# Performance work log

Hardware: AMD Instinct MI355X
Metric: run time of the kernel (lower is better)

Reference implementation:

```python
import jax, jax.numpy as jnp
import numpy as np

H = 32          # num_attention_heads
HD = 128        # head_dim
HID = H * HD    # hidden_size = 4096
KB_LEN = 1024   # number of KB entries
TOPK = 128      # top_k_kb (dynamic_sparsify=True)
ROPE_THETA = 10000.0
PAD = -1000000000.0  # PADDING_VALUE


def rope_cos_sin(position_ids, head_dim, theta):
    inv_freq = 1.0 / (theta ** (jnp.arange(0, head_dim, 2, dtype=jnp.float32) / head_dim))
    freqs = position_ids.astype(jnp.float32)[..., None] * inv_freq  # [B,q,hd/2]
    emb = jnp.concatenate([freqs, freqs], axis=-1)                  # [B,q,hd]
    return jnp.cos(emb), jnp.sin(emb)


def rotate_half(x):
    half = x.shape[-1] // 2
    return jnp.concatenate([-x[..., half:], x[..., :half]], axis=-1)


def apply_rope(q, k, cos, sin):
    cos = cos[:, None]  # [B,1,q,hd]
    sin = sin[:, None]
    return q * cos + rotate_half(q) * sin, k * cos + rotate_half(k) * sin


def setup_inputs() -> dict:
    key = jax.random.key(0)
    ks = jax.random.split(key, 9)
    B, Q = 1, 2048
    w_scale = 0.02  # keep activations numerically sane
    hidden_states = jax.random.normal(ks[0], (B, Q, HID), jnp.float32)
    causal = jnp.where(jnp.tril(jnp.ones((Q, Q), bool)), 0.0, PAD).astype(jnp.float32)
    attention_mask = jnp.broadcast_to(causal[None, None], (B, 1, Q, Q))
    position_ids = jnp.broadcast_to(jnp.arange(Q)[None], (B, Q))
    kb_keys = jax.random.normal(ks[1], (KB_LEN, HID), jnp.float32)
    kb_values = jax.random.normal(ks[2], (KB_LEN, HID), jnp.float32)
    Wq = jax.random.normal(ks[3], (HID, HID), jnp.float32) * w_scale
    Wq2 = jax.random.normal(ks[4], (HID, HID), jnp.float32) * w_scale
    Wk = jax.random.normal(ks[5], (HID, HID), jnp.float32) * w_scale
    Wv = jax.random.normal(ks[6], (HID, HID), jnp.float32) * w_scale
    Wo = jax.random.normal(ks[7], (HID, HID), jnp.float32) * w_scale
    score_shift = jnp.zeros((H, 1), jnp.float32) - 3.0
    return {"hidden_states": hidden_states, "attention_mask": attention_mask,
            "position_ids": position_ids, "kb_keys": kb_keys, "kb_values": kb_values,
            "Wq": Wq, "Wq2": Wq2, "Wk": Wk, "Wv": Wv, "Wo": Wo,
            "score_shift": score_shift}


def kblam_attention(hidden_states, attention_mask, position_ids, kb_keys, kb_values,
                    Wq, Wq2, Wk, Wv, Wo, score_shift):
    B, Q, _ = hidden_states.shape
    scale = 1.0 / np.sqrt(HD)

    def heads(x):  # [B,Q,HID] -> [B,H,Q,HD]
        return x.reshape(B, Q, H, HD).transpose(0, 2, 1, 3)

    q = heads(hidden_states @ Wq.T)
    q2 = heads(hidden_states @ Wq2.T)   # second query head (used for KB top-k pruning)
    k = heads(hidden_states @ Wk.T)
    v = heads(hidden_states @ Wv.T)

    cos, sin = rope_cos_sin(position_ids, HD, ROPE_THETA)
    q, k = apply_rope(q, k, cos, sin)   # num_kv_groups == 1, repeat_kv is identity

    # --- KB path: [kb_len, H*HD] -> [B,H,kb_len,HD] ---
    kbk = jnp.broadcast_to(kb_keys.reshape(KB_LEN, H, HD).transpose(1, 0, 2)[None], (B, H, KB_LEN, HD))
    kbv = jnp.broadcast_to(kb_values.reshape(KB_LEN, H, HD).transpose(1, 0, 2)[None], (B, H, KB_LEN, HD))

    # prune_key_value (dynamic_sparsify): top-k KB rows by summed q2-scores
    aw2 = jnp.einsum('bhqd,bhkd->bhqk', q2, kbk) * scale          # [B,H,Q,KB_LEN]
    idx = jax.lax.stop_gradient(jax.lax.top_k(aw2.sum((1, 2)), TOPK)[1])  # [B,TOPK]
    gidx = jnp.broadcast_to(idx[:, None, :, None], (B, H, TOPK, HD))
    kbk = jnp.take_along_axis(kbk, gidx, axis=2)                  # [B,H,TOPK,HD]
    kbv = jnp.take_along_axis(kbv, gidx, axis=2)
    kb_len = TOPK

    k_all = jnp.concatenate([kbk, k], axis=2)                     # [B,H,kb_len+Q,HD]
    v_all = jnp.concatenate([kbv, v], axis=2)

    # kb attention mask: zeros, except fully-padded query rows get PADDING_VALUE
    padding_mask = jnp.all(attention_mask < 0, axis=-1, keepdims=True)  # [B,1,Q,1]
    kb_mask = jnp.where(padding_mask, PAD, 0.0).astype(attention_mask.dtype)
    mask = jnp.concatenate([jnp.broadcast_to(kb_mask, (B, 1, Q, kb_len)), attention_mask], axis=-1)

    attn = jnp.einsum('bhqd,bhkd->bhqk', q, k_all) * scale
    # learned per-head shift on KB scores (score_shift: [H,1], init -3)
    attn = attn.at[..., :kb_len].add(score_shift.reshape(1, H, 1, 1))
    attn = attn + mask
    attn = jax.nn.softmax(attn.astype(jnp.float32), axis=-1).astype(q.dtype)

    out = jnp.einsum('bhqk,bhkd->bhqd', attn, v_all)              # [B,H,Q,HD]
    out = out.transpose(0, 2, 1, 3).reshape(B, Q, HID)
    return out @ Wo.T


def reference(hidden_states, attention_mask, position_ids, kb_keys, kb_values,
              Wq, Wq2, Wk, Wv, Wo, score_shift):
    return kblam_attention(hidden_states, attention_mask, position_ids, kb_keys, kb_values,
                           Wq, Wq2, Wk, Wv, Wo, score_shift)
```

## Files before the change

### kernel.cpp

```cpp
#include <hip/hip_runtime.h>
#include <stdint.h>
#include <stddef.h>

#define NH 32
#define HD 128
#define HID 4096
#define QLEN 2048
#define KBLEN 1024
#define NTOPK 128
#define KVLEN 2176
#define PADV -1e9f
#define SCALE 0.08838834764831845f
#define LOG2E 1.4426950408889634f
#define SC2 (SCALE * LOG2E)
#define DEFER_THR 8.0f

typedef __attribute__((ext_vector_type(4))) float f32x4;
typedef __attribute__((ext_vector_type(4))) unsigned short u16x4;
typedef __attribute__((ext_vector_type(8))) short s16x8;

typedef const __attribute__((address_space(1))) void* gas1_t;
typedef __attribute__((address_space(3))) void* las3_t;

__device__ __forceinline__ void gload_lds16(const void* g, void* l) {
  __builtin_amdgcn_global_load_lds((gas1_t)g, (las3_t)l, 16, 0, 0);
}

__device__ __forceinline__ unsigned short f2bf(float x) {
  union { float f; unsigned u; } z; z.f = x;
  unsigned r = z.u + 0x7fffu + ((z.u >> 16) & 1u);
  return (unsigned short)(r >> 16);
}


__global__ void k_cast(const float* __restrict__ src, unsigned short* __restrict__ dst, int n4) {
  int i = blockIdx.x * 256 + threadIdx.x;
  if (i >= n4) return;
  f32x4 v = ((const f32x4*)src)[i];
  u16x4 o;
  o[0] = f2bf(v[0]); o[1] = f2bf(v[1]); o[2] = f2bf(v[2]); o[3] = f2bf(v[3]);
  ((u16x4*)dst)[i] = o;
}

__global__ void k_rowsum_p(const float* __restrict__ x, float* __restrict__ part) {
  int d = blockIdx.x * 256 + threadIdx.x;
  int q0 = blockIdx.y * 128;
  float acc = 0.f;
  for (int q = q0; q < q0 + 128; ++q) acc += x[(size_t)q * HID + d];
  part[(size_t)blockIdx.y * HID + d] = acc;
}
__global__ void k_rowsum_r(const float* __restrict__ part, float* __restrict__ out) {
  int d = blockIdx.x * 256 + threadIdx.x;
  float acc = 0.f;
#pragma unroll
  for (int i = 0; i < 16; ++i) acc += part[(size_t)i * HID + d];
  out[d] = acc;
}

__global__ void k_dotrows(const float* __restrict__ vec, const float* __restrict__ mat,
                          float* __restrict__ out, int K, float s) {
  int n = blockIdx.x * 4 + (threadIdx.x >> 6);
  int lane = threadIdx.x & 63;
  const float* row = mat + (size_t)n * K;
  float acc = 0.f;
  for (int j = lane; j < K; j += 64) acc += vec[j] * row[j];
#pragma unroll
  for (int off = 32; off > 0; off >>= 1) acc += __shfl_down(acc, off, 64);
  if (lane == 0) out[n] = acc * s;
}

__global__ void k_topk(const float* __restrict__ scores, int* __restrict__ idx) {
  __shared__ float s[KBLEN];
  int t = threadIdx.x;
  s[t] = scores[t];
  __syncthreads();
  float mine = s[t];
  int rank = 0;
  for (int j = 0; j < KBLEN; ++j) {
    float v = s[j];
    rank += (v > mine) || (v == mine && j < t);
  }
  if (rank < NTOPK) idx[rank] = t;
}

__global__ void k_cs(const int* __restrict__ pos_ids, float2* __restrict__ cs) {
  int t = blockIdx.x * 256 + threadIdx.x;
  int p = t >> 6, i = t & 63;
  float pos = (float)pos_ids[p];
  float invf = powf(10000.0f, -(float)i / 64.0f);
  float a = pos * invf;
  cs[p * 64 + i] = make_float2(cosf(a), sinf(a));
}

__global__ void k_gather(const float* __restrict__ kbk, const float* __restrict__ kbv,
                         const int* __restrict__ idx,
                         unsigned short* __restrict__ kall, unsigned short* __restrict__ vallT) {
  int t = blockIdx.x * 256 + threadIdx.x;
  int d = t & 127;
  int i = (t >> 7) & 127;
  int hh = t >> 14;
  int kr = idx[i];
  size_t src = (size_t)kr * HID + hh * HD + d;
  kall[((size_t)hh * KVLEN + i) * HD + d] = f2bf(kbk[src]);
  vallT[((size_t)hh * HD + d) * KVLEN + i] = f2bf(kbv[src]);
}

#define GBK 64
#define ABUF 8192
#define BBUF 16384
#define BUFE (ABUF + BBUF)

template<int MODE>
__global__ __launch_bounds__(512)
void gemm_bt(const unsigned short* __restrict__ A, const unsigned short* __restrict__ B,
             float* __restrict__ Cf, unsigned short* __restrict__ Cb,
             int M, int N, int K, int RH, int RO, const float2* __restrict__ cs2,
             float qsc) {
  __shared__ unsigned short lds[3 * BUFE];
  const int tid = threadIdx.x;
  const int lane = tid & 63;
  const int wave = tid >> 6;
  const int lo = lane & 15, hi = lane >> 4;
  const int wm = wave >> 2, wn = wave & 3;

  const int nwg = gridDim.x * gridDim.y;
  const int orig = blockIdx.y * gridDim.x + blockIdx.x;
  const int wg = (orig & 7) * (nwg >> 3) + (orig >> 3);
  const int bx = wg % gridDim.x, by = wg / gridDim.x;
  const int m0 = by * 128, n0 = bx * 256;

  auto stageA = [&](int kt, int bufe, int g) {
    int j0 = g * 512 + wave * 64;
    int j = j0 + lane;
    int row = j >> 3, cb = j & 7;
    gload_lds16(A + (size_t)(m0 + row) * K + kt * GBK + ((cb ^ (row & 7)) << 3),
                (void*)(lds + bufe + j0 * 8));
  };
  auto stageB = [&](int kt, int bufe, int g) {
    int j0 = g * 512 + wave * 64;
    int j = j0 + lane;
    int row = j >> 3, cb = j & 7;
    gload_lds16(B + (size_t)(n0 + row) * K + kt * GBK + ((cb ^ (row & 7)) << 3),
                (void*)(lds + bufe + ABUF + j0 * 8));
  };

  f32x4 acc[4][4] = {};

  stageA(0, 0, 0); stageA(0, 0, 1);
  stageB(0, 0, 0); stageB(0, 0, 1); stageB(0, 0, 2); stageB(0, 0, 3);
  stageA(1, BUFE, 0); stageA(1, BUFE, 1);
  stageB(1, BUFE, 0); stageB(1, BUFE, 1); stageB(1, BUFE, 2); stageB(1, BUFE, 3);

  const int NT = K / GBK;
  const int sa = (lo & 7) << 3;
  const int bbase = (wn >> 1) * 128 + (wn & 1) * 32;
  int bi = 0;

  for (int kt = 0; kt < NT; ++kt) {
    if (kt < NT - 1) { asm volatile("s_waitcnt vmcnt(6)" ::: "memory"); }
    else             { asm volatile("s_waitcnt vmcnt(0)" ::: "memory"); }
    __builtin_amdgcn_sched_barrier(0);
    __builtin_amdgcn_s_barrier();
    __builtin_amdgcn_sched_barrier(0);

    const int bufe = bi * BUFE;
    const int nbufe = ((bi + 2 >= 3) ? bi - 1 : bi + 2) * BUFE;
    const bool pre = (kt + 2 < NT);
    const unsigned short* Ab = lds + bufe;
    const unsigned short* Bb = lds + bufe + ABUF;
    const int arow = wm * 64 + lo;
    const int brow = bbase + lo;

    s16x8 af[4], b01[2], b23[2];
    const int c0 = (hi * 8) ^ sa;
    const int c1 = (32 + hi * 8) ^ sa;

#pragma unroll
    for (int i = 0; i < 4; ++i) af[i] = *(const s16x8*)(Ab + (arow + i * 16) * 64 + c0);
    b01[0] = *(const s16x8*)(Bb + (brow +  0) * 64 + c0);
    b01[1] = *(const s16x8*)(Bb + (brow + 16) * 64 + c0);
    if (pre) { stageA(kt + 2, nbufe, 0); stageA(kt + 2, nbufe, 1); }
    asm volatile("s_waitcnt lgkmcnt(0)" ::: "memory");
    __builtin_amdgcn_sched_barrier(0);
    __builtin_amdgcn_s_setprio(1);
#pragma unroll
    for (int i = 0; i < 4; ++i) {
      acc[i][0] = __builtin_amdgcn_mfma_f32_16x16x32_bf16(af[i], b01[0], acc[i][0], 0, 0, 0);
      acc[i][1] = __builtin_amdgcn_mfma_f32_16x16x32_bf16(af[i], b01[1], acc[i][1], 0, 0, 0);
    }
    __builtin_amdgcn_s_setprio(0);

    b23[0] = *(const s16x8*)(Bb + (brow + 64) * 64 + c0);
    b23[1] = *(const s16x8*)(Bb + (brow + 80) * 64 + c0);
    if (pre) { stageB(kt + 2, nbufe, 0); stageB(kt + 2, nbufe, 1); }
    asm volatile("s_waitcnt lgkmcnt(0)" ::: "memory");
    __builtin_amdgcn_sched_barrier(0);
    __builtin_amdgcn_s_setprio(1);
#pragma unroll
    for (int i = 0; i < 4; ++i) {
      acc[i][2] = __builtin_amdgcn_mfma_f32_16x16x32_bf16(af[i], b23[0], acc[i][2], 0, 0, 0);
      acc[i][3] = __builtin_amdgcn_mfma_f32_16x16x32_bf16(af[i], b23[1], acc[i][3], 0, 0, 0);
    }
    __builtin_amdgcn_s_setprio(0);

#pragma unroll
    for (int i = 0; i < 4; ++i) af[i] = *(const s16x8*)(Ab + (arow + i * 16) * 64 + c1);
    b01[0] = *(const s16x8*)(Bb + (brow +  0) * 64 + c1);
    b01[1] = *(const s16x8*)(Bb + (brow + 16) * 64 + c1);
    if (pre) { stageB(kt + 2, nbufe, 2); stageB(kt + 2, nbufe, 3); }
    asm volatile("s_waitcnt lgkmcnt(0)" ::: "memory");
    __builtin_amdgcn_sched_barrier(0);
    __builtin_amdgcn_s_setprio(1);
#pragma unroll
    for (int i = 0; i < 4; ++i) {
      acc[i][0] = __builtin_amdgcn_mfma_f32_16x16x32_bf16(af[i], b01[0], acc[i][0], 0, 0, 0);
      acc[i][1] = __builtin_amdgcn_mfma_f32_16x16x32_bf16(af[i], b01[1], acc[i][1], 0, 0, 0);
    }
    __builtin_amdgcn_s_setprio(0);

    b23[0] = *(const s16x8*)(Bb + (brow + 64) * 64 + c1);
    b23[1] = *(const s16x8*)(Bb + (brow + 80) * 64 + c1);
    asm volatile("s_waitcnt lgkmcnt(0)" ::: "memory");
    __builtin_amdgcn_sched_barrier(0);
    __builtin_amdgcn_s_setprio(1);
#pragma unroll
    for (int i = 0; i < 4; ++i) {
      acc[i][2] = __builtin_amdgcn_mfma_f32_16x16x32_bf16(af[i], b23[0], acc[i][2], 0, 0, 0);
      acc[i][3] = __builtin_amdgcn_mfma_f32_16x16x32_bf16(af[i], b23[1], acc[i][3], 0, 0, 0);
    }
    __builtin_amdgcn_s_setprio(0);

    bi = (bi + 1 == 3) ? 0 : bi + 1;
  }

  if (MODE == 2) {
#pragma unroll
    for (int i = 0; i < 4; ++i) {
#pragma unroll
      for (int j = 0; j < 2; ++j) {
#pragma unroll
        for (int r = 0; r < 4; ++r) {
          int row = m0 + wm * 64 + i * 16 + hi * 4 + r;
          int col = n0 + bbase + j * 16 + lo;
          int hh = col >> 7, d = col & 127;
          float2 cp = cs2[row * 64 + d];
          float x1 = acc[i][j][r] * qsc, x2 = acc[i][j + 2][r] * qsc;
          size_t base = ((size_t)hh * RH + RO + row) * HD;
          Cb[base + d]      = f2bf(x1 * cp.x - x2 * cp.y);
          Cb[base + d + 64] = f2bf(x2 * cp.x + x1 * cp.y);
        }
      }
    }
  } else if (MODE == 3) {
#pragma unroll
    for (int i = 0; i < 4; ++i) {
#pragma unroll
      for (int j = 0; j < 4; ++j) {
        int rowb = m0 + wm * 64 + i * 16 + hi * 4;
        int col = n0 + bbase + (j >> 1) * 64 + (j & 1) * 16 + lo;
        int hh = col >> 7, d = col & 127;
        u16x4 o4;
#pragma unroll
        for (int r = 0; r < 4; ++r) o4[r] = f2bf(acc[i][j][r]);
        *(u16x4*)(Cb + ((size_t)hh * HD + d) * RH + RO + rowb) = o4;
      }
    }
  } else {
#pragma unroll
    for (int i = 0; i < 4; ++i) {
#pragma unroll
      for (int j = 0; j < 4; ++j) {
#pragma unroll
        for (int r = 0; r < 4; ++r) {
          int row = m0 + wm * 64 + i * 16 + hi * 4 + r;
          int col = n0 + bbase + (j >> 1) * 64 + (j & 1) * 16 + lo;
          float v = acc[i][j][r];
          if (MODE == 0) {
            Cf[(size_t)row * N + col] = v;
          } else {
            int hh = col >> 7, d = col & 127;
            Cb[((size_t)hh * RH + RO + row) * HD + d] = f2bf(v);
          }
        }
      }
    }
  }
}

__global__ __launch_bounds__(256)
void attn_kernel(const unsigned short* __restrict__ qh,
                 const unsigned short* __restrict__ kall,
                 const unsigned short* __restrict__ vallT,
                 const float* __restrict__ sshift,
                 unsigned short* __restrict__ ctx) {
  __shared__ __align__(1024) unsigned short Ks[64 * 128];
  __shared__ __align__(1024) unsigned short Vs[128 * 64];
  __shared__ __align__(16)  unsigned short Plds[4][16 * 72];

  int orig = blockIdx.y * 32 + blockIdx.x;
  int wgid = (orig & 7) * 128 + (orig >> 3);
  int h = wgid >> 5;
  int qc = 31 - (wgid & 31);

  const int tid = threadIdx.x;
  const int lane = tid & 63;
  const int wave = tid >> 6;
  const int lo = lane & 15;
  const int hi = lane >> 4;
  const float shiftL = sshift[h] * LOG2E;

  const unsigned short* kb = kall + (size_t)h * KVLEN * HD;
  const unsigned short* vtb = vallT + (size_t)h * HD * KVLEN;

  const int m0 = qc * 64;
  const int nt = qc + 3;
  const int qrow = m0 + wave * 16 + hi * 4;

  s16x8 qf[4];
  {
    const unsigned short* qp = qh + ((size_t)h * QLEN + m0 + wave * 16 + lo) * HD + hi * 8;
#pragma unroll
    for (int kc = 0; kc < 4; ++kc) qf[kc] = *(const s16x8*)(qp + kc * 32);
  }

  float m_run[4], l_part[4];
#pragma unroll
  for (int r = 0; r < 4; ++r) { m_run[r] = -1e30f; l_part[r] = 0.f; }
  f32x4 o[8] = {};

  for (int kt = 0; kt < nt; ++kt) {
    const unsigned short* kg = kb + (size_t)kt * 64 * HD;
    const unsigned short* vg = vtb + kt * 64;
    __syncthreads();
#pragma unroll
    for (int it = 0; it < 4; ++it) {
      int j0 = it * 256 + wave * 64;
      int j = j0 + lane;
      int row = j >> 4, cb = j & 15;
      gload_lds16(kg + row * 128 + ((cb ^ (row & 7)) * 8), (void*)(Ks + j0 * 8));
      int d = j >> 3, c = j & 7;
      gload_lds16(vg + (size_t)d * KVLEN + ((c ^ (d & 7)) << 3), (void*)(Vs + j0 * 8));
    }
    __syncthreads();

    f32x4 s[4] = {};
#pragma unroll
    for (int kc = 0; kc < 4; ++kc) {
#pragma unroll
      for (int g = 0; g < 4; ++g) {
        int key = g * 16 + lo;
        s16x8 kf = *(const s16x8*)(Ks + key * 128 + (((kc * 4 + hi) ^ (key & 7)) * 8));
        s[g] = __builtin_amdgcn_mfma_f32_16x16x32_bf16(qf[kc], kf, s[g], 0, 0, 0);
      }
    }

    if (kt < 2) {
#pragma unroll
      for (int g = 0; g < 4; ++g)
#pragma unroll
        for (int r = 0; r < 4; ++r) s[g][r] += shiftL;
    } else if (kt == nt - 1) {
      const int kvbase = kt * 64;
#pragma unroll
      for (int r = 0; r < 4; ++r) {
        int qr = qrow + r;
#pragma unroll
        for (int g = 0; g < 4; ++g) {
          int kv = kvbase + g * 16 + lo;
          s[g][r] = (kv - NTOPK > qr) ? PADV : s[g][r];
        }
      }
    }

    float mx[4];
    bool need = false;
#pragma unroll
    for (int r = 0; r < 4; ++r) {
      mx[r] = fmaxf(fmaxf(s[0][r], s[1][r]), fmaxf(s[2][r], s[3][r]));
      need = need || (mx[r] > m_run[r] + DEFER_THR);
    }
    if (__any((int)need)) {
#pragma unroll
      for (int off = 1; off < 16; off <<= 1)
#pragma unroll
        for (int r = 0; r < 4; ++r) mx[r] = fmaxf(mx[r], __shfl_xor(mx[r], off, 64));
#pragma unroll
      for (int r = 0; r < 4; ++r) {
        float mn = fmaxf(m_run[r], mx[r]);
        float alpha = __builtin_amdgcn_exp2f(m_run[r] - mn);
        m_run[r] = mn;
        l_part[r] *= alpha;
#pragma unroll
        for (int db = 0; db < 8; ++db) o[db][r] *= alpha;
      }
    }

#pragma unroll
    for (int r = 0; r < 4; ++r) {
#pragma unroll
      for (int g = 0; g < 4; ++g) {
        float p = __builtin_amdgcn_exp2f(s[g][r] - m_run[r]);
        l_part[r] += p;
        Plds[wave][(hi * 4 + r) * 72 + g * 16 + lo] = f2bf(p);
      }
    }

    s16x8 pf0 = *(const s16x8*)(&Plds[wave][lo * 72 + hi * 8]);
    s16x8 pf1 = *(const s16x8*)(&Plds[wave][lo * 72 + 32 + hi * 8]);
#pragma unroll
    for (int db = 0; db < 8; ++db) {
      int d = db * 16 + lo;
      s16x8 vf0 = *(const s16x8*)(Vs + d * 64 + ((hi       ^ (d & 7)) << 3));
      s16x8 vf1 = *(const s16x8*)(Vs + d * 64 + (((4 + hi) ^ (d & 7)) << 3));
      o[db] = __builtin_amdgcn_mfma_f32_16x16x32_bf16(pf0, vf0, o[db], 0, 0, 0);
      o[db] = __builtin_amdgcn_mfma_f32_16x16x32_bf16(pf1, vf1, o[db], 0, 0, 0);
    }
  }

#pragma unroll
  for (int off = 1; off < 16; off <<= 1)
#pragma unroll
    for (int r = 0; r < 4; ++r) l_part[r] += __shfl_xor(l_part[r], off, 64);

  float rinv[4];
#pragma unroll
  for (int r = 0; r < 4; ++r) rinv[r] = __builtin_amdgcn_rcpf(l_part[r]);

#pragma unroll
  for (int db = 0; db < 8; ++db) {
#pragma unroll
    for (int r = 0; r < 4; ++r) {
      int row = qrow + r;
      int col = h * HD + db * 16 + lo;
      ctx[(size_t)row * HID + col] = f2bf(o[db][r] * rinv[r]);
    }
  }
}


extern "C" void kernel_launch(void* const* d_in, const int* in_sizes, int n_in,
                              void* d_out, int out_size, void* d_ws, size_t ws_size,
                              hipStream_t stream) {
  const float* hidden    = (const float*)d_in[0];
  const int*   pos       = (const int*)d_in[2];
  const float* kb_keys   = (const float*)d_in[3];
  const float* kb_values = (const float*)d_in[4];
  const float* Wq        = (const float*)d_in[5];
  const float* Wq2       = (const float*)d_in[6];
  const float* Wk        = (const float*)d_in[7];
  const float* Wv        = (const float*)d_in[8];
  const float* Wo        = (const float*)d_in[9];
  const float* sshift    = (const float*)d_in[10];
  float* out = (float*)d_out;

  char* ws = (char*)d_ws;
  size_t off = 0;
  auto alloc = [&](size_t bytes) { char* p = ws + off; off += (bytes + 255) & ~(size_t)255; return p; };
  unsigned short* hidden_bf = (unsigned short*)alloc((size_t)QLEN * HID * 2);
  unsigned short* wbuf      = (unsigned short*)alloc((size_t)HID * HID * 2);
  unsigned short* qbf       = (unsigned short*)alloc((size_t)NH * QLEN * HD * 2);
  unsigned short* kallp     = (unsigned short*)alloc((size_t)NH * KVLEN * HD * 2);
  unsigned short* vallT     = (unsigned short*)alloc((size_t)NH * HD * KVLEN * 2);
  unsigned short* ctx       = (unsigned short*)alloc((size_t)QLEN * HID * 2);
  float2*         cs2       = (float2*)alloc((size_t)QLEN * 64 * 8);
  float*          part      = (float*)alloc((size_t)16 * HID * 4);
  float*          hsum      = (float*)alloc(HID * 4);
  float*          qs        = (float*)alloc(HID * 4);
  float*          scores    = (float*)alloc(KBLEN * 4);
  int*            idx       = (int*)alloc(NTOPK * 4);

  dim3 blk(256);

  k_cast<<<QLEN * HID / 4 / 256, blk, 0, stream>>>(hidden, hidden_bf, QLEN * HID / 4);
  k_rowsum_p<<<dim3(HID / 256, 16), blk, 0, stream>>>(hidden, part);
  k_rowsum_r<<<HID / 256, blk, 0, stream>>>(part, hsum);
  k_dotrows<<<HID / 4, blk, 0, stream>>>(hsum, Wq2, qs, HID, 1.0f);
  k_dotrows<<<KBLEN / 4, blk, 0, stream>>>(qs, kb_keys, scores, HID, SCALE);
  k_topk<<<1, KBLEN, 0, stream>>>(scores, idx);
  k_cs<<<QLEN * 64 / 256, blk, 0, stream>>>(pos, cs2);

  dim3 ggrid(HID / 256, QLEN / 128);
  dim3 gblk(512);
  int wcast_blocks = HID * HID / 4 / 256;

  k_cast<<<wcast_blocks, blk, 0, stream>>>(Wq, wbuf, HID * HID / 4);
  gemm_bt<2><<<ggrid, gblk, 0, stream>>>(hidden_bf, wbuf, nullptr, qbf, QLEN, HID, HID, QLEN, 0, cs2, (float)SC2);
  k_cast<<<wcast_blocks, blk, 0, stream>>>(Wk, wbuf, HID * HID / 4);
  gemm_bt<2><<<ggrid, gblk, 0, stream>>>(hidden_bf, wbuf, nullptr, kallp, QLEN, HID, HID, KVLEN, NTOPK, cs2, 1.0f);
  k_cast<<<wcast_blocks, blk, 0, stream>>>(Wv, wbuf, HID * HID / 4);
  gemm_bt<3><<<ggrid, gblk, 0, stream>>>(hidden_bf, wbuf, nullptr, vallT, QLEN, HID, HID, KVLEN, NTOPK, cs2, 1.0f);

  k_gather<<<NH * NTOPK * HD / 256, blk, 0, stream>>>(kb_keys, kb_values, idx, kallp, vallT);

  dim3 agrid(32, NH);
  attn_kernel<<<agrid, blk, 0, stream>>>(qbf, kallp, vallT, sshift, ctx);

  k_cast<<<wcast_blocks, blk, 0, stream>>>(Wo, wbuf, HID * HID / 4);
  gemm_bt<0><<<ggrid, gblk, 0, stream>>>(ctx, wbuf, out, nullptr, QLEN, HID, HID, 0, 0, cs2, 1.0f);
}
```

Before: 566.3 us.

## Double attention query tile per block to 128 rows, two row groups per wave

The attention kernel now processes 128 query rows per workgroup instead of 64. Each wave handles two 16-row groups, so every K/V tile loaded into LDS is reused by twice as many query rows, halving global K/V traffic and barrier count per query. Waves skip diagonal tiles that are fully masked for them, and the P scratch buffer gets an XOR swizzle to reduce LDS bank conflicts. The trade-off is half as many workgroups (512), more registers per wave that may lower occupancy, and worse load balance across the causal triangle.

```diff
diff --git a/kernel.cpp b/kernel.cpp
--- a/kernel.cpp
+++ b/kernel.cpp
@@ -295,12 +295,12 @@
                  unsigned short* __restrict__ ctx) {
   __shared__ __align__(1024) unsigned short Ks[64 * 128];
   __shared__ __align__(1024) unsigned short Vs[128 * 64];
-  __shared__ __align__(16)  unsigned short Plds[4][16 * 72];
-
-  int orig = blockIdx.y * 32 + blockIdx.x;
-  int wgid = (orig & 7) * 128 + (orig >> 3);
-  int h = wgid >> 5;
-  int qc = 31 - (wgid & 31);
+  __shared__ __align__(16)  unsigned short Plds[4][32 * 72];
+
+  int orig = blockIdx.y * 16 + blockIdx.x;
+  int wgid = (orig & 7) * 64 + (orig >> 3);
+  int h = wgid >> 4;
+  int qc = 15 - (wgid & 15);
 
   const int tid = threadIdx.x;
   const int lane = tid & 63;
@@ -312,21 +312,26 @@
   const unsigned short* kb = kall + (size_t)h * KVLEN * HD;
   const unsigned short* vtb = vallT + (size_t)h * HD * KVLEN;
 
-  const int m0 = qc * 64;
-  const int nt = qc + 3;
-  const int qrow = m0 + wave * 16 + hi * 4;
-
-  s16x8 qf[4];
-  {
-    const unsigned short* qp = qh + ((size_t)h * QLEN + m0 + wave * 16 + lo) * HD + hi * 8;
-#pragma unroll
-    for (int kc = 0; kc < 4; ++kc) qf[kc] = *(const s16x8*)(qp + kc * 32);
+  const int m0 = qc * 128;
+  const int nt = 2 * qc + 4;
+  const int diagkt = nt - 2 + (wave >> 1);
+
+  s16x8 qf[2][4];
+#pragma unroll
+  for (int qg = 0; qg < 2; ++qg) {
+    const unsigned short* qp = qh + ((size_t)h * QLEN + m0 + wave * 32 + qg * 16 + lo) * HD + hi * 8;
+#pragma unroll
+    for (int kc = 0; kc < 4; ++kc) qf[qg][kc] = *(const s16x8*)(qp + kc * 32);
   }
 
-  float m_run[4], l_part[4];
-#pragma unroll
-  for (int r = 0; r < 4; ++r) { m_run[r] = -1e30f; l_part[r] = 0.f; }
-  f32x4 o[8] = {};
+  float m_run[2][4], l_part[2][4];
+#pragma unroll
+  for (int qg = 0; qg < 2; ++qg)
+#pragma unroll
+    for (int r = 0; r < 4; ++r) { m_run[qg][r] = -1e30f; l_part[qg][r] = 0.f; }
+  f32x4 o[2][8] = {};
+
+  const int rkey = ((lo >> 2) & 3) << 4;
 
   for (int kt = 0; kt < nt; ++kt) {
     const unsigned short* kg = kb + (size_t)kt * 64 * HD;
@@ -334,105 +339,137 @@
     __syncthreads();
 #pragma unroll
     for (int it = 0; it < 4; ++it) {
-      int j0 = it * 256 + wave * 64;
-      int j = j0 + lane;
+      int j0 = it * 256 + tid - lane + lane;
+      int j = it * 256 + tid;
+      int jw = it * 256 + wave * 64;
       int row = j >> 4, cb = j & 15;
-      gload_lds16(kg + row * 128 + ((cb ^ (row & 7)) * 8), (void*)(Ks + j0 * 8));
+      gload_lds16(kg + row * 128 + ((cb ^ (row & 7)) * 8), (void*)(Ks + jw * 8));
       int d = j >> 3, c = j & 7;
-      gload_lds16(vg + (size_t)d * KVLEN + ((c ^ (d & 7)) << 3), (void*)(Vs + j0 * 8));
+      gload_lds16(vg + (size_t)d * KVLEN + ((c ^ (d & 7)) << 3), (void*)(Vs + jw * 8));
+      (void)j0;
     }
     __syncthreads();
 
-    f32x4 s[4] = {};
-#pragma unroll
-    for (int kc = 0; kc < 4; ++kc) {
-#pragma unroll
-      for (int g = 0; g < 4; ++g) {
-        int key = g * 16 + lo;
-        s16x8 kf = *(const s16x8*)(Ks + key * 128 + (((kc * 4 + hi) ^ (key & 7)) * 8));
-        s[g] = __builtin_amdgcn_mfma_f32_16x16x32_bf16(qf[kc], kf, s[g], 0, 0, 0);
-      }
-    }
-
-    if (kt < 2) {
-#pragma unroll
-      for (int g = 0; g < 4; ++g)
-#pragma unroll
-        for (int r = 0; r < 4; ++r) s[g][r] += shiftL;
-    } else if (kt == nt - 1) {
-      const int kvbase = kt * 64;
+    if (kt <= diagkt) {
+      f32x4 s[2][4] = {};
+#pragma unroll
+      for (int kc = 0; kc < 4; ++kc) {
+#pragma unroll
+        for (int kgi = 0; kgi < 4; ++kgi) {
+          int key = kgi * 16 + lo;
+          s16x8 kf = *(const s16x8*)(Ks + key * 128 + (((kc * 4 + hi) ^ (key & 7)) * 8));
+          s[0][kgi] = __builtin_amdgcn_mfma_f32_16x16x32_bf16(qf[0][kc], kf, s[0][kgi], 0, 0, 0);
+          s[1][kgi] = __builtin_amdgcn_mfma_f32_16x16x32_bf16(qf[1][kc], kf, s[1][kgi], 0, 0, 0);
+        }
+      }
+
+      if (kt < 2) {
+#pragma unroll
+        for (int qg = 0; qg < 2; ++qg)
+#pragma unroll
+          for (int kgi = 0; kgi < 4; ++kgi)
+#pragma unroll
+            for (int r = 0; r < 4; ++r) s[qg][kgi][r] += shiftL;
+      } else if (kt >= nt - 2) {
+        const int kvbase = kt * 64 - NTOPK;
+#pragma unroll
+        for (int qg = 0; qg < 2; ++qg) {
+#pragma unroll
+          for (int r = 0; r < 4; ++r) {
+            int qr = m0 + wave * 32 + qg * 16 + hi * 4 + r;
+#pragma unroll
+            for (int kgi = 0; kgi < 4; ++kgi) {
+              int kv = kvbase + kgi * 16 + lo;
+              s[qg][kgi][r] = (kv > qr) ? PADV : s[qg][kgi][r];
+            }
+          }
+        }
+      }
+
+      float mx[2][4];
+      bool need = false;
+#pragma unroll
+      for (int qg = 0; qg < 2; ++qg)
+#pragma unroll
+        for (int r = 0; r < 4; ++r) {
+          mx[qg][r] = fmaxf(fmaxf(s[qg][0][r], s[qg][1][r]), fmaxf(s[qg][2][r], s[qg][3][r]));
+          need = need || (mx[qg][r] > m_run[qg][r] + DEFER_THR);
+        }
+      if (__any((int)need)) {
+#pragma unroll
+        for (int off = 1; off < 16; off <<= 1)
+#pragma unroll
+          for (int qg = 0; qg < 2; ++qg)
+#pragma unroll
+            for (int r = 0; r < 4; ++r) mx[qg][r] = fmaxf(mx[qg][r], __shfl_xor(mx[qg][r], off, 64));
+#pragma unroll
+        for (int qg = 0; qg < 2; ++qg)
+#pragma unroll
+          for (int r = 0; r < 4; ++r) {
+            float mn = fmaxf(m_run[qg][r], mx[qg][r]);
+            float alpha = __builtin_amdgcn_exp2f(m_run[qg][r] - mn);
+            m_run[qg][r] = mn;
+            l_part[qg][r] *= alpha;
+#pragma unroll
+            for (int db = 0; db < 8; ++db) o[qg][db][r] *= alpha;
+          }
+      }
+
+#pragma unroll
+      for (int qg = 0; qg < 2; ++qg) {
+#pragma unroll
+        for (int r = 0; r < 4; ++r) {
+#pragma unroll
+          for (int kgi = 0; kgi < 4; ++kgi) {
+            float p = __builtin_amdgcn_exp2f(s[qg][kgi][r] - m_run[qg][r]);
+            l_part[qg][r] += p;
+            Plds[wave][(qg * 16 + hi * 4 + r) * 72 + ((kgi * 16 + lo) ^ (hi << 4))] = f2bf(p);
+          }
+        }
+      }
+
+      s16x8 pf[2][2];
+#pragma unroll
+      for (int qg = 0; qg < 2; ++qg) {
+        pf[qg][0] = *(const s16x8*)(&Plds[wave][(qg * 16 + lo) * 72 + ((hi * 8) ^ rkey)]);
+        pf[qg][1] = *(const s16x8*)(&Plds[wave][(qg * 16 + lo) * 72 + ((32 + hi * 8) ^ rkey)]);
+      }
+#pragma unroll
+      for (int db = 0; db < 8; ++db) {
+        int d = db * 16 + lo;
+        s16x8 vf0 = *(const s16x8*)(Vs + d * 64 + ((hi       ^ (d & 7)) << 3));
+        s16x8 vf1 = *(const s16x8*)(Vs + d * 64 + (((4 + hi) ^ (d & 7)) << 3));
+        o[0][db] = __builtin_amdgcn_mfma_f32_16x16x32_bf16(pf[0][0], vf0, o[0][db], 0, 0, 0);
+        o[0][db] = __builtin_amdgcn_mfma_f32_16x16x32_bf16(pf[0][1], vf1, o[0][db], 0, 0, 0);
+        o[1][db] = __builtin_amdgcn_mfma_f32_16x16x32_bf16(pf[1][0], vf0, o[1][db], 0, 0, 0);
+        o[1][db] = __builtin_amdgcn_mfma_f32_16x16x32_bf16(pf[1][1], vf1, o[1][db], 0, 0, 0);
+      }
+    }
+  }
+
+#pragma unroll
+  for (int off = 1; off < 16; off <<= 1)
+#pragma unroll
+    for (int qg = 0; qg < 2; ++qg)
+#pragma unroll
+      for (int r = 0; r < 4; ++r) l_part[qg][r] += __shfl_xor(l_part[qg][r], off, 64);
+
+  float rinv[2][4];
+#pragma unroll
+  for (int qg = 0; qg < 2; ++qg)
+#pragma unroll
+    for (int r = 0; r < 4; ++r) rinv[qg][r] = __builtin_amdgcn_rcpf(l_part[qg][r]);
+
+#pragma unroll
+  for (int qg = 0; qg < 2; ++qg) {
+#pragma unroll
+    for (int db = 0; db < 8; ++db) {
 #pragma unroll
       for (int r = 0; r < 4; ++r) {
-        int qr = qrow + r;
-#pragma unroll
-        for (int g = 0; g < 4; ++g) {
-          int kv = kvbase + g * 16 + lo;
-          s[g][r] = (kv - NTOPK > qr) ? PADV : s[g][r];
-        }
-      }
-    }
-
-    float mx[4];
-    bool need = false;
-#pragma unroll
-    for (int r = 0; r < 4; ++r) {
-      mx[r] = fmaxf(fmaxf(s[0][r], s[1][r]), fmaxf(s[2][r], s[3][r]));
-      need = need || (mx[r] > m_run[r] + DEFER_THR);
-    }
-    if (__any((int)need)) {
-#pragma unroll
-      for (int off = 1; off < 16; off <<= 1)
-#pragma unroll
-        for (int r = 0; r < 4; ++r) mx[r] = fmaxf(mx[r], __shfl_xor(mx[r], off, 64));
-#pragma unroll
-      for (int r = 0; r < 4; ++r) {
-        float mn = fmaxf(m_run[r], mx[r]);
-        float alpha = __builtin_amdgcn_exp2f(m_run[r] - mn);
-        m_run[r] = mn;
-        l_part[r] *= alpha;
-#pragma unroll
-        for (int db = 0; db < 8; ++db) o[db][r] *= alpha;
-      }
-    }
-
-#pragma unroll
-    for (int r = 0; r < 4; ++r) {
-#pragma unroll
-      for (int g = 0; g < 4; ++g) {
-        float p = __builtin_amdgcn_exp2f(s[g][r] - m_run[r]);
-        l_part[r] += p;
-        Plds[wave][(hi * 4 + r) * 72 + g * 16 + lo] = f2bf(p);
-      }
-    }
-
-    s16x8 pf0 = *(const s16x8*)(&Plds[wave][lo * 72 + hi * 8]);
-    s16x8 pf1 = *(const s16x8*)(&Plds[wave][lo * 72 + 32 + hi * 8]);
-#pragma unroll
-    for (int db = 0; db < 8; ++db) {
-      int d = db * 16 + lo;
-      s16x8 vf0 = *(const s16x8*)(Vs + d * 64 + ((hi       ^ (d & 7)) << 3));
-      s16x8 vf1 = *(const s16x8*)(Vs + d * 64 + (((4 + hi) ^ (d & 7)) << 3));
-      o[db] = __builtin_amdgcn_mfma_f32_16x16x32_bf16(pf0, vf0, o[db], 0, 0, 0);
-      o[db] = __builtin_amdgcn_mfma_f32_16x16x32_bf16(pf1, vf1, o[db], 0, 0, 0);
-    }
-  }
-
-#pragma unroll
-  for (int off = 1; off < 16; off <<= 1)
-#pragma unroll
-    for (int r = 0; r < 4; ++r) l_part[r] += __shfl_xor(l_part[r], off, 64);
-
-  float rinv[4];
-#pragma unroll
-  for (int r = 0; r < 4; ++r) rinv[r] = __builtin_amdgcn_rcpf(l_part[r]);
-
-#pragma unroll
-  for (int db = 0; db < 8; ++db) {
-#pragma unroll
-    for (int r = 0; r < 4; ++r) {
-      int row = qrow + r;
-      int col = h * HD + db * 16 + lo;
-      ctx[(size_t)row * HID + col] = f2bf(o[db][r] * rinv[r]);
+        int row = m0 + wave * 32 + qg * 16 + hi * 4 + r;
+        int col = h * HD + db * 16 + lo;
+        ctx[(size_t)row * HID + col] = f2bf(o[qg][db][r] * rinv[qg][r]);
+      }
     }
   }
 }
@@ -492,7 +529,7 @@
 
   k_gather<<<NH * NTOPK * HD / 256, blk, 0, stream>>>(kb_keys, kb_values, idx, kallp, vallT);
 
-  dim3 agrid(32, NH);
+  dim3 agrid(16, NH);
   attn_kernel<<<agrid, blk, 0, stream>>>(qbf, kallp, vallT, sshift, ctx);
 
   k_cast<<<wcast_blocks, blk, 0, stream>>>(Wo, wbuf, HID * HID / 4);
```

Result: slower. 604.7 us (+6.8%).

## Fuse fp32-to-bf16 weight cast into GEMM B-operand staging

Applied to the files above, without the earlier changes.

Removes the four separate weight-cast kernels. The GEMM now reads fp32 weights directly through registers, packs them to bf16 with v_cvt_pk_bf16_f32, and writes them into LDS, pipelined one k-tile ahead. This drops a full write and re-read of each 32 MB bf16 weight copy. In exchange, the GEMM reads twice the B bytes from global memory, uses more registers, replaces async LDS DMA with VGPR round-trips, and changes the vmcnt accounting.

```diff
diff --git a/kernel.cpp b/kernel.cpp
--- a/kernel.cpp
+++ b/kernel.cpp
@@ -17,6 +17,7 @@
 
 typedef __attribute__((ext_vector_type(4))) float f32x4;
 typedef __attribute__((ext_vector_type(4))) unsigned short u16x4;
+typedef __attribute__((ext_vector_type(4))) unsigned u32x4;
 typedef __attribute__((ext_vector_type(8))) short s16x8;
 
 typedef const __attribute__((address_space(1))) void* gas1_t;
@@ -30,6 +31,12 @@
   union { float f; unsigned u; } z; z.f = x;
   unsigned r = z.u + 0x7fffu + ((z.u >> 16) & 1u);
   return (unsigned short)(r >> 16);
+}
+
+__device__ __forceinline__ unsigned cvt_pk_bf16(float s0, float s1) {
+  unsigned d;
+  asm volatile("v_cvt_pk_bf16_f32 %0, %1, %2" : "=v"(d) : "v"(s0), "v"(s1));
+  return d;
 }
 
 
@@ -112,7 +119,7 @@
 
 template<int MODE>
 __global__ __launch_bounds__(512)
-void gemm_bt(const unsigned short* __restrict__ A, const unsigned short* __restrict__ B,
+void gemm_bt(const unsigned short* __restrict__ A, const float* __restrict__ B,
              float* __restrict__ Cf, unsigned short* __restrict__ Cb,
              int M, int N, int K, int RH, int RO, const float2* __restrict__ cs2,
              float qsc) {
@@ -136,20 +143,39 @@
     gload_lds16(A + (size_t)(m0 + row) * K + kt * GBK + ((cb ^ (row & 7)) << 3),
                 (void*)(lds + bufe + j0 * 8));
   };
-  auto stageB = [&](int kt, int bufe, int g) {
-    int j0 = g * 512 + wave * 64;
-    int j = j0 + lane;
-    int row = j >> 3, cb = j & 7;
-    gload_lds16(B + (size_t)(n0 + row) * K + kt * GBK + ((cb ^ (row & 7)) << 3),
-                (void*)(lds + bufe + ABUF + j0 * 8));
+
+  f32x4 breg[8];
+  auto loadB = [&](int kt) {
+#pragma unroll
+    for (int c = 0; c < 4; ++c) {
+      int j = tid * 4 + c;
+      int row = j >> 3, cb = j & 7;
+      const float* src = B + (size_t)(n0 + row) * K + kt * GBK + ((cb ^ (row & 7)) << 3);
+      breg[c * 2]     = *(const f32x4*)(src);
+      breg[c * 2 + 1] = *(const f32x4*)(src + 4);
+    }
   };
+  auto writeB = [&](int bufe, int c) {
+    int j = tid * 4 + c;
+    u32x4 u;
+    f32x4 v0 = breg[c * 2], v1 = breg[c * 2 + 1];
+    u[0] = cvt_pk_bf16(v0[0], v0[1]);
+    u[1] = cvt_pk_bf16(v0[2], v0[3]);
+    u[2] = cvt_pk_bf16(v1[0], v1[1]);
+    u[3] = cvt_pk_bf16(v1[2], v1[3]);
+    *(u32x4*)(lds + bufe + ABUF + j * 8) = u;
+  };
 
   f32x4 acc[4][4] = {};
 
+  loadB(0);
   stageA(0, 0, 0); stageA(0, 0, 1);
-  stageB(0, 0, 0); stageB(0, 0, 1); stageB(0, 0, 2); stageB(0, 0, 3);
+  asm volatile("s_waitcnt vmcnt(2)" ::: "memory");
+#pragma unroll
+  for (int c = 0; c < 4; ++c) writeB(0, c);
   stageA(1, BUFE, 0); stageA(1, BUFE, 1);
-  stageB(1, BUFE, 0); stageB(1, BUFE, 1); stageB(1, BUFE, 2); stageB(1, BUFE, 3);
+  loadB(1);
+  asm volatile("s_waitcnt lgkmcnt(0)" ::: "memory");
 
   const int NT = K / GBK;
   const int sa = (lo & 7) << 3;
@@ -157,15 +183,16 @@
   int bi = 0;
 
   for (int kt = 0; kt < NT; ++kt) {
-    if (kt < NT - 1) { asm volatile("s_waitcnt vmcnt(6)" ::: "memory"); }
-    else             { asm volatile("s_waitcnt vmcnt(0)" ::: "memory"); }
+    asm volatile("s_waitcnt vmcnt(10)" ::: "memory");
     __builtin_amdgcn_sched_barrier(0);
     __builtin_amdgcn_s_barrier();
     __builtin_amdgcn_sched_barrier(0);
 
     const int bufe = bi * BUFE;
-    const int nbufe = ((bi + 2 >= 3) ? bi - 1 : bi + 2) * BUFE;
+    const int nbufe  = ((bi + 2 >= 3) ? bi - 1 : bi + 2) * BUFE;
+    const int wbufe  = ((bi + 1 >= 3) ? bi - 2 : bi + 1) * BUFE;
     const bool pre = (kt + 2 < NT);
+    const bool wnext = (kt + 1 < NT);
     const unsigned short* Ab = lds + bufe;
     const unsigned short* Bb = lds + bufe + ABUF;
     const int arow = wm * 64 + lo;
@@ -180,6 +207,7 @@
     b01[0] = *(const s16x8*)(Bb + (brow +  0) * 64 + c0);
     b01[1] = *(const s16x8*)(Bb + (brow + 16) * 64 + c0);
     if (pre) { stageA(kt + 2, nbufe, 0); stageA(kt + 2, nbufe, 1); }
+    if (wnext) { writeB(wbufe, 0); writeB(wbufe, 1); }
     asm volatile("s_waitcnt lgkmcnt(0)" ::: "memory");
     __builtin_amdgcn_sched_barrier(0);
     __builtin_amdgcn_s_setprio(1);
@@ -192,7 +220,7 @@
 
     b23[0] = *(const s16x8*)(Bb + (brow + 64) * 64 + c0);
     b23[1] = *(const s16x8*)(Bb + (brow + 80) * 64 + c0);
-    if (pre) { stageB(kt + 2, nbufe, 0); stageB(kt + 2, nbufe, 1); }
+    if (wnext) { writeB(wbufe, 2); writeB(wbufe, 3); }
     asm volatile("s_waitcnt lgkmcnt(0)" ::: "memory");
     __builtin_amdgcn_sched_barrier(0);
     __builtin_amdgcn_s_setprio(1);
@@ -207,7 +235,7 @@
     for (int i = 0; i < 4; ++i) af[i] = *(const s16x8*)(Ab + (arow + i * 16) * 64 + c1);
     b01[0] = *(const s16x8*)(Bb + (brow +  0) * 64 + c1);
     b01[1] = *(const s16x8*)(Bb + (brow + 16) * 64 + c1);
-    if (pre) { stageB(kt + 2, nbufe, 2); stageB(kt + 2, nbufe, 3); }
+    if (pre) loadB(kt + 2);
     asm volatile("s_waitcnt lgkmcnt(0)" ::: "memory");
     __builtin_amdgcn_sched_barrier(0);
     __builtin_amdgcn_s_setprio(1);
@@ -457,7 +485,6 @@
   size_t off = 0;
   auto alloc = [&](size_t bytes) { char* p = ws + off; off += (bytes + 255) & ~(size_t)255; return p; };
   unsigned short* hidden_bf = (unsigned short*)alloc((size_t)QLEN * HID * 2);
-  unsigned short* wbuf      = (unsigned short*)alloc((size_t)HID * HID * 2);
   unsigned short* qbf       = (unsigned short*)alloc((size_t)NH * QLEN * HD * 2);
   unsigned short* kallp     = (unsigned short*)alloc((size_t)NH * KVLEN * HD * 2);
   unsigned short* vallT     = (unsigned short*)alloc((size_t)NH * HD * KVLEN * 2);
@@ -481,20 +508,15 @@
 
   dim3 ggrid(HID / 256, QLEN / 128);
   dim3 gblk(512);
-  int wcast_blocks = HID * HID / 4 / 256;
-
-  k_cast<<<wcast_blocks, blk, 0, stream>>>(Wq, wbuf, HID * HID / 4);
-  gemm_bt<2><<<ggrid, gblk, 0, stream>>>(hidden_bf, wbuf, nullptr, qbf, QLEN, HID, HID, QLEN, 0, cs2, (float)SC2);
-  k_cast<<<wcast_blocks, blk, 0, stream>>>(Wk, wbuf, HID * HID / 4);
-  gemm_bt<2><<<ggrid, gblk, 0, stream>>>(hidden_bf, wbuf, nullptr, kallp, QLEN, HID, HID, KVLEN, NTOPK, cs2, 1.0f);
-  k_cast<<<wcast_blocks, blk, 0, stream>>>(Wv, wbuf, HID * HID / 4);
-  gemm_bt<3><<<ggrid, gblk, 0, stream>>>(hidden_bf, wbuf, nullptr, vallT, QLEN, HID, HID, KVLEN, NTOPK, cs2, 1.0f);
+
+  gemm_bt<2><<<ggrid, gblk, 0, stream>>>(hidden_bf, Wq, nullptr, qbf, QLEN, HID, HID, QLEN, 0, cs2, (float)SC2);
+  gemm_bt<2><<<ggrid, gblk, 0, stream>>>(hidden_bf, Wk, nullptr, kallp, QLEN, HID, HID, KVLEN, NTOPK, cs2, 1.0f);
+  gemm_bt<3><<<ggrid, gblk, 0, stream>>>(hidden_bf, Wv, nullptr, vallT, QLEN, HID, HID, KVLEN, NTOPK, cs2, 1.0f);
 
   k_gather<<<NH * NTOPK * HD / 256, blk, 0, stream>>>(kb_keys, kb_values, idx, kallp, vallT);
 
   dim3 agrid(32, NH);
   attn_kernel<<<agrid, blk, 0, stream>>>(qbf, kallp, vallT, sshift, ctx);
 
-  k_cast<<<wcast_blocks, blk, 0, stream>>>(Wo, wbuf, HID * HID / 4);
-  gemm_bt<0><<<ggrid, gblk, 0, stream>>>(ctx, wbuf, out, nullptr, QLEN, HID, HID, 0, 0, cs2, 1.0f);
-}
+  gemm_bt<0><<<ggrid, gblk, 0, stream>>>(ctx, Wo, out, nullptr, QLEN, HID, HID, 0, 0, cs2, 1.0f);
+}
```

Measured after the change: 979.6 us. 73.0% more time.
